# Performance work log

Hardware: AMD Instinct MI355X
Metric: run time of the kernel (lower is better)

The kernel has to match this reference:

```python
import jax, jax.numpy as jnp
import numpy as np

B, C, H, W = 4, 256, 64, 64
C8 = C // 8


def setup_inputs() -> dict:
    key = jax.random.key(0)
    ks = jax.random.split(key, 7)
    return {
        "x": jax.random.normal(ks[0], (B, C, H, W), dtype=jnp.float32),
        "Wq": jax.random.normal(ks[1], (C8, C), dtype=jnp.float32) * 0.05,
        "bq": jax.random.normal(ks[2], (C8,), dtype=jnp.float32) * 0.05,
        "Wk": jax.random.normal(ks[3], (C8, C), dtype=jnp.float32) * 0.05,
        "bk": jax.random.normal(ks[4], (C8,), dtype=jnp.float32) * 0.05,
        "Wv": jax.random.normal(ks[5], (C, C), dtype=jnp.float32) * 0.05,
        "bv": jax.random.normal(ks[6], (C,), dtype=jnp.float32) * 0.05,
        "gamma": jnp.zeros((1,), dtype=jnp.float32),
    }


def reference(x, Wq, bq, Wk, bk, Wv, bv, gamma):
    b, c, h, w = x.shape
    n = h * w
    xf = x.reshape(b, c, n)  # [B, C, N]
    # 1x1 convs == per-pixel linear maps over channels
    q = jnp.einsum('oc,bcn->bon', Wq, xf) + bq[None, :, None]  # [B, C/8, N]
    k = jnp.einsum('oc,bcn->bon', Wk, xf) + bk[None, :, None]  # [B, C/8, N]
    v = jnp.einsum('oc,bcn->bon', Wv, xf) + bv[None, :, None]  # [B, C, N]
    # s[b,i,j] = q_i . k_j ; torch softmax over dim=-2 (the i axis)
    s = jnp.einsum('bci,bcj->bij', q, k)  # [B, N, N]
    attn_T = jax.nn.softmax(s, axis=-2)
    # o[b,c,j] = sum_i v[b,c,i] * attn_T[b,i,j]
    o = jnp.einsum('bci,bij->bcj', v, attn_T)  # [B, C, N]
    return x + gamma[0] * o.reshape(b, c, h, w)
```

## Files before the change

### kernel.cpp

```cpp
#include <hip/hip_runtime.h>
#include <hip/hip_bf16.h>


typedef float  f32x16 __attribute__((ext_vector_type(16)));
typedef float  f32x4  __attribute__((ext_vector_type(4)));
typedef short  s16x8  __attribute__((ext_vector_type(8)));
typedef unsigned int u32;
typedef unsigned int u32x4 __attribute__((ext_vector_type(4)));

__device__ __forceinline__ s16x8 ld16(const ushort* p) {
  return *reinterpret_cast<const s16x8*>(p);
}
__device__ __forceinline__ ushort f2bf(float f) {
  return (ushort)((__float_as_uint(f) + 0x8000u) >> 16);
}
__device__ __forceinline__ u32 cvt_pk_bf16(float lo, float hi) {
  u32 r;
  asm("v_cvt_pk_bf16_f32 %0, %1, %2" : "=v"(r) : "v"(lo), "v"(hi));
  return r;
}

__global__ void wf_kernel(const float* __restrict__ Wq, const float* __restrict__ Wk,
                          const float* __restrict__ Wv,
                          const float* __restrict__ bq, const float* __restrict__ bk,
                          const float* __restrict__ bv, ushort* __restrict__ WF) {
  const int blk = blockIdx.x;
  const int ob = blk / 17, kb = blk % 17;
  const int t = threadIdx.x;
  const int l = t >> 3, e = t & 7;
  const int l31 = l & 31, g = l >> 5;
  const int o = ob * 32 + l31;
  float val;
  if (kb == 16) {
    float bias = (ob == 0) ? bq[l31] : (ob == 1) ? bk[l31] : bv[o - 64];
    val = (g == 0 && e == 0) ? bias : 0.f;
  } else {
    const int c = kb * 16 + (e & 3) + ((e >> 2) << 3) + (g << 2);
    val = (ob == 0) ? Wq[l31 * 256 + c]
        : (ob == 1) ? Wk[l31 * 256 + c]
                    : Wv[(o - 64) * 256 + c];
  }
  WF[((size_t)blk * 64 + l) * 8 + e] = f2bf(val);
}

__global__ __launch_bounds__(640) void proj_kernel(
    const float* __restrict__ x, const ushort* __restrict__ WF,
    ushort* __restrict__ qA, ushort* __restrict__ kB, ushort* __restrict__ vA) {
  __shared__ ushort xbf[17 * 1024];
  __shared__ ushort obuf[20480];
  const int bid = blockIdx.x;
  const int b = bid >> 6, w = bid & 63;
  const int n0 = w << 6;
  const int t = threadIdx.x;

  const float* xb = x + (size_t)(b * 256) * 4096 + n0;
  #pragma unroll
  for (int kk = 0; kk < 7; ++kk) {
    int idx = t + kk * 640;
    if (idx < 4096) {
      int c = idx >> 4, nq = idx & 15;
      f32x4 xv = *reinterpret_cast<const f32x4*>(xb + (size_t)c * 4096 + nq * 4);
      int kb = c >> 4, r = c & 15;
      int gg = (r >> 2) & 1, ee = (r & 3) + ((r >> 3) << 2);
      #pragma unroll
      for (int u = 0; u < 4; ++u) {
        int n = nq * 4 + u;
        xbf[kb * 1024 + ((n >> 5) * 2 + gg) * 256 + (n & 31) * 8 + ee] = f2bf(xv[u]);
      }
    }
  }
  for (int u = t; u < 1024; u += 640) {
    int gg = (u >> 8) & 1, ee = u & 7;
    xbf[16 * 1024 + u] = (gg == 0 && ee == 0) ? (ushort)0x3F80 : (ushort)0;
  }
  __syncthreads();

  const int l = t & 63;
  const int wv = __builtin_amdgcn_readfirstlane(t >> 6);
  const int l31 = l & 31, g = l >> 5;

  s16x8 wf[17];
  #pragma unroll
  for (int kb = 0; kb < 17; ++kb)
    wf[kb] = ld16(WF + ((size_t)(wv * 17 + kb) * 64 + l) * 8);

  f32x16 acc[2];
  #pragma unroll
  for (int nb = 0; nb < 2; ++nb)
    #pragma unroll
    for (int r = 0; r < 16; ++r) acc[nb][r] = 0.f;

  #pragma unroll
  for (int nb = 0; nb < 2; ++nb)
    #pragma unroll
    for (int kb = 0; kb < 17; ++kb)
      acc[nb] = __builtin_amdgcn_mfma_f32_32x32x16_bf16(
          wf[kb], ld16(xbf + kb * 1024 + (nb * 2 + g) * 256 + l31 * 8), acc[nb], 0, 0, 0);

  if (wv < 2) {
    const int obase = wv * 2048;
    #pragma unroll
    for (int nb = 0; nb < 2; ++nb)
      #pragma unroll
      for (int r = 0; r < 16; ++r)
        obuf[obase + (nb * 4 + (r >> 3) * 2 + g) * 256 + l31 * 8 + (r & 3) + (((r >> 2) & 1) << 2)]
            = f2bf(acc[nb][r]);
  } else {
    const int gv = (l31 >> 2) & 1;
    const int ev = (l31 & 3) + (((l31 >> 3) & 1) << 2);
    #pragma unroll
    for (int nb = 0; nb < 2; ++nb) {
      const int fi = (nb * 2 + (l31 >> 4)) * 2 + gv;
      #pragma unroll
      for (int r = 0; r < 16; ++r) {
        const int c = (wv - 2) * 32 + (r & 3) + ((r >> 2) << 3) + (g << 2);
        obuf[4096 + (fi * 256 + c) * 8 + ev] = f2bf(acc[nb][r]);
      }
    }
  }
  __syncthreads();

  const size_t qbase = (size_t)(b * 64 + w) * 2048;
  const size_t vbase = ((size_t)b * 512 + w * 8) * 2048;
  #pragma unroll
  for (int kk = 0; kk < 4; ++kk) {
    int ci = t + kk * 640;
    int off = ci * 8;
    s16x8 val = ld16(obuf + off);
    ushort* dst = (off < 2048) ? (qA + qbase + off)
                : (off < 4096) ? (kB + qbase + off - 2048)
                               : (vA + vbase + off - 4096);
    *reinterpret_cast<s16x8*>(dst) = val;
  }
}

__global__ __launch_bounds__(512, 2) void attn_kernel(
    const ushort* __restrict__ qA, const ushort* __restrict__ kB, const ushort* __restrict__ vA,
    const float* __restrict__ x, const float* __restrict__ gamma, float* __restrict__ out) {
  __shared__ ushort pls[2 * 8 * 2 * 512];
  __shared__ float lsr[4][2][64];
  const int bid = blockIdx.x;
  const int b = bid & 3;
  const int jt = bid >> 2;
  const int j0 = jt << 6;
  const int t = threadIdx.x;
  const int l = t & 63;
  const int wv = __builtin_amdgcn_readfirstlane(t >> 6);
  const int l31 = l & 31, g = l >> 5;
  const float gm = gamma[0];

  if (wv >= 4) {
    const int sw = wv - 4;
    s16x8 kf00, kf01, kf10, kf11;
    {
      const size_t kb0 = (size_t)((b * 64 + jt) * 8 + g) * 256 + l31 * 8;
      kf00 = ld16(kB + kb0);
      kf01 = ld16(kB + kb0 + 512);
      kf10 = ld16(kB + kb0 + 1024);
      kf11 = ld16(kB + kb0 + 1536);
    }
    float lsum0 = 1e-30f, lsum1 = 1e-30f;
    s16x8 qf0, qf1;
    {
      const size_t qb = (size_t)((b * 64 + (sw >> 1)) * 8 + (sw & 1) * 4 + g) * 256 + l31 * 8;
      qf0 = ld16(qA + qb);
      qf1 = ld16(qA + qb + 512);
    }
    for (int reg = 0; reg <= 32; ++reg) {
      if (reg < 32) {
        const int wi = reg, buf = wi & 1;
        f32x16 s0, s1;
        #pragma unroll
        for (int r = 0; r < 16; ++r) { s0[r] = 0.f; s1[r] = 0.f; }
        s0 = __builtin_amdgcn_mfma_f32_32x32x16_bf16(qf0, kf00, s0, 0, 0, 0);
        s0 = __builtin_amdgcn_mfma_f32_32x32x16_bf16(qf1, kf01, s0, 0, 0, 0);
        s1 = __builtin_amdgcn_mfma_f32_32x32x16_bf16(qf0, kf10, s1, 0, 0, 0);
        s1 = __builtin_amdgcn_mfma_f32_32x32x16_bf16(qf1, kf11, s1, 0, 0, 0);
        if (wi < 31) {
          const size_t qb = (size_t)((b * 64 + (wi + 1) * 2 + (sw >> 1)) * 8 + (sw & 1) * 4 + g) * 256 + l31 * 8;
          qf0 = ld16(qA + qb);
          qf1 = ld16(qA + qb + 512);
        }
        float p0[16], p1[16], ls0 = 0.f, ls1 = 0.f;
        #pragma unroll
        for (int r = 0; r < 16; ++r) {
          p0[r] = __builtin_amdgcn_exp2f(__builtin_fmaf(s0[r], 1.4426950408889634f, -24.0f));
          p1[r] = __builtin_amdgcn_exp2f(__builtin_fmaf(s1[r], 1.4426950408889634f, -24.0f));
          ls0 += p0[r];
          ls1 += p1[r];
        }
        lsum0 += ls0;
        lsum1 += ls1;
        u32x4 w00, w01, w10, w11;
        #pragma unroll
        for (int q = 0; q < 4; ++q) {
          w00[q] = cvt_pk_bf16(p0[2 * q],     p0[2 * q + 1]);
          w01[q] = cvt_pk_bf16(p0[8 + 2 * q], p0[8 + 2 * q + 1]);
          w10[q] = cvt_pk_bf16(p1[2 * q],     p1[2 * q + 1]);
          w11[q] = cvt_pk_bf16(p1[8 + 2 * q], p1[8 + 2 * q + 1]);
        }
        ushort* p00 = pls + ((buf * 16 + (2 * sw + 0) * 2 + 0) * 512) + l * 8;
        ushort* p01 = pls + ((buf * 16 + (2 * sw + 1) * 2 + 0) * 512) + l * 8;
        ushort* p10 = pls + ((buf * 16 + (2 * sw + 0) * 2 + 1) * 512) + l * 8;
        ushort* p11 = pls + ((buf * 16 + (2 * sw + 1) * 2 + 1) * 512) + l * 8;
        *reinterpret_cast<s16x8*>(p00) = __builtin_bit_cast(s16x8, w00);
        *reinterpret_cast<s16x8*>(p01) = __builtin_bit_cast(s16x8, w01);
        *reinterpret_cast<s16x8*>(p10) = __builtin_bit_cast(s16x8, w10);
        *reinterpret_cast<s16x8*>(p11) = __builtin_bit_cast(s16x8, w11);
      } else {
        lsr[sw][0][l] = lsum0;
        lsr[sw][1][l] = lsum1;
      }
      asm volatile("s_waitcnt lgkmcnt(0)" ::: "memory");
      __builtin_amdgcn_s_barrier();
      __builtin_amdgcn_sched_barrier(0);
    }
  } else {
    const int pv = wv;
    const ushort* vbase = vA + ((size_t)(b * 512 + g) * 256 + pv * 64 + l31) * 8;
    f32x16 acc[2][2];
    #pragma unroll
    for (int cg = 0; cg < 2; ++cg)
      #pragma unroll
      for (int jb = 0; jb < 2; ++jb)
        #pragma unroll
        for (int r = 0; r < 16; ++r) acc[cg][jb][r] = 0.f;
    s16x8 vf[8][2];
    for (int reg = 0; reg <= 32; ++reg) {
      if (reg == 0) {
        #pragma unroll
        for (int m = 0; m < 8; ++m) {
          vf[m][0] = ld16(vbase + (size_t)m * 4096);
          vf[m][1] = ld16(vbase + (size_t)m * 4096 + 256);
        }
      } else {
        const int wi = reg - 1, buf = wi & 1;
        __builtin_amdgcn_s_setprio(1);
        #pragma unroll
        for (int m = 0; m < 8; ++m) {
          s16x8 pf0 = ld16(pls + ((buf * 16 + m * 2 + 0) * 512) + l * 8);
          s16x8 pf1 = ld16(pls + ((buf * 16 + m * 2 + 1) * 512) + l * 8);
          acc[0][0] = __builtin_amdgcn_mfma_f32_32x32x16_bf16(vf[m][0], pf0, acc[0][0], 0, 0, 0);
          acc[1][0] = __builtin_amdgcn_mfma_f32_32x32x16_bf16(vf[m][1], pf0, acc[1][0], 0, 0, 0);
          acc[0][1] = __builtin_amdgcn_mfma_f32_32x32x16_bf16(vf[m][0], pf1, acc[0][1], 0, 0, 0);
          acc[1][1] = __builtin_amdgcn_mfma_f32_32x32x16_bf16(vf[m][1], pf1, acc[1][1], 0, 0, 0);
          if (reg < 32) {
            vf[m][0] = ld16(vbase + (size_t)(reg * 8 + m) * 4096);
            vf[m][1] = ld16(vbase + (size_t)(reg * 8 + m) * 4096 + 256);
          }
        }
        __builtin_amdgcn_s_setprio(0);
      }
      __builtin_amdgcn_s_barrier();
      __builtin_amdgcn_sched_barrier(0);
    }
    #pragma unroll
    for (int jb = 0; jb < 2; ++jb) {
      float tot = 0.f;
      #pragma unroll
      for (int sw2 = 0; sw2 < 4; ++sw2)
        tot += lsr[sw2][jb][l31] + lsr[sw2][jb][l31 + 32];
      const float sc = gm / tot;
      #pragma unroll
      for (int cg = 0; cg < 2; ++cg) {
        #pragma unroll
        for (int r = 0; r < 16; ++r) {
          const int c = pv * 64 + cg * 32 + (r & 3) + ((r >> 2) << 3) + (g << 2);
          const size_t idx = (size_t)(b * 256 + c) * 4096 + j0 + jb * 32 + l31;
          out[idx] = __builtin_fmaf(sc, acc[cg][jb][r], x[idx]);
        }
      }
    }
  }
}

extern "C" void kernel_launch(void* const* d_in, const int* in_sizes, int n_in,
                              void* d_out, int out_size, void* d_ws, size_t ws_size,
                              hipStream_t stream) {
  const float* x     = (const float*)d_in[0];
  const float* Wq    = (const float*)d_in[1];
  const float* bq    = (const float*)d_in[2];
  const float* Wk    = (const float*)d_in[3];
  const float* bk    = (const float*)d_in[4];
  const float* Wv    = (const float*)d_in[5];
  const float* bv    = (const float*)d_in[6];
  const float* gamma = (const float*)d_in[7];
  float* out = (float*)d_out;

  char* ws = (char*)d_ws;
  ushort* WF = (ushort*)(ws);
  ushort* qA = (ushort*)(ws + 262144);
  ushort* kB = (ushort*)(ws + 262144 + 1048576);
  ushort* vA = (ushort*)(ws + 262144 + 2097152);

  wf_kernel  <<<170, 512, 0, stream>>>(Wq, Wk, Wv, bq, bk, bv, WF);
  proj_kernel<<<256, 640, 0, stream>>>(x, WF, qA, kB, vA);
  attn_kernel<<<256, 512, 0, stream>>>(qA, kB, vA, x, gamma, out);
}
```

Baseline: 63.97 us.

## Prefetch residual x tile into LDS by softmax waves; batch P fragment loads

The softmax-producer waves now load the residual x tile for the block's 64 columns across all 256 channels during the last iterations of their loop and stage it in a new 64KB LDS buffer. The PV waves' epilogue then reads x from LDS instead of issuing strided global loads after the main loop. Separately, all 16 P fragments are loaded from LDS into registers before the MFMA sequence rather than interleaved with it. This hides epilogue global latency behind compute, at the cost of much more LDS per block (which may limit the two-blocks-per-CU occupancy) and higher register pressure.

```diff
diff --git a/kernel.cpp b/kernel.cpp
--- a/kernel.cpp
+++ b/kernel.cpp
@@ -138,7 +138,8 @@
     const ushort* __restrict__ qA, const ushort* __restrict__ kB, const ushort* __restrict__ vA,
     const float* __restrict__ x, const float* __restrict__ gamma, float* __restrict__ out) {
   __shared__ ushort pls[2 * 8 * 2 * 512];
-  __shared__ float lsr[4][2][64];
+  __shared__ float  xls[256 * 64];
+  __shared__ float  lsr[4][2][64];
   const int bid = blockIdx.x;
   const int b = bid & 3;
   const int jt = bid >> 2;
@@ -166,7 +167,21 @@
       qf0 = ld16(qA + qb);
       qf1 = ld16(qA + qb + 512);
     }
+    const float* xrow = x + (size_t)(b * 256) * 4096 + j0 + l;
+    float xr[8];
     for (int reg = 0; reg <= 32; ++reg) {
+      if (reg >= 25) {
+        const int cw0 = (reg - 25) * 32 + sw * 8;
+        #pragma unroll
+        for (int rr = 0; rr < 8; ++rr)
+          xls[(cw0 + rr) * 64 + l] = xr[rr];
+      }
+      if (reg >= 24 && reg < 32) {
+        const int cl0 = (reg - 24) * 32 + sw * 8;
+        #pragma unroll
+        for (int rr = 0; rr < 8; ++rr)
+          xr[rr] = xrow[(size_t)(cl0 + rr) * 4096];
+      }
       if (reg < 32) {
         const int wi = reg, buf = wi & 1;
         f32x16 s0, s1;
@@ -235,15 +250,19 @@
         }
       } else {
         const int wi = reg - 1, buf = wi & 1;
+        s16x8 pf[8][2];
+        #pragma unroll
+        for (int m = 0; m < 8; ++m) {
+          pf[m][0] = ld16(pls + ((buf * 16 + m * 2 + 0) * 512) + l * 8);
+          pf[m][1] = ld16(pls + ((buf * 16 + m * 2 + 1) * 512) + l * 8);
+        }
         __builtin_amdgcn_s_setprio(1);
         #pragma unroll
         for (int m = 0; m < 8; ++m) {
-          s16x8 pf0 = ld16(pls + ((buf * 16 + m * 2 + 0) * 512) + l * 8);
-          s16x8 pf1 = ld16(pls + ((buf * 16 + m * 2 + 1) * 512) + l * 8);
-          acc[0][0] = __builtin_amdgcn_mfma_f32_32x32x16_bf16(vf[m][0], pf0, acc[0][0], 0, 0, 0);
-          acc[1][0] = __builtin_amdgcn_mfma_f32_32x32x16_bf16(vf[m][1], pf0, acc[1][0], 0, 0, 0);
-          acc[0][1] = __builtin_amdgcn_mfma_f32_32x32x16_bf16(vf[m][0], pf1, acc[0][1], 0, 0, 0);
-          acc[1][1] = __builtin_amdgcn_mfma_f32_32x32x16_bf16(vf[m][1], pf1, acc[1][1], 0, 0, 0);
+          acc[0][0] = __builtin_amdgcn_mfma_f32_32x32x16_bf16(vf[m][0], pf[m][0], acc[0][0], 0, 0, 0);
+          acc[1][0] = __builtin_amdgcn_mfma_f32_32x32x16_bf16(vf[m][1], pf[m][0], acc[1][0], 0, 0, 0);
+          acc[0][1] = __builtin_amdgcn_mfma_f32_32x32x16_bf16(vf[m][0], pf[m][1], acc[0][1], 0, 0, 0);
+          acc[1][1] = __builtin_amdgcn_mfma_f32_32x32x16_bf16(vf[m][1], pf[m][1], acc[1][1], 0, 0, 0);
           if (reg < 32) {
             vf[m][0] = ld16(vbase + (size_t)(reg * 8 + m) * 4096);
             vf[m][1] = ld16(vbase + (size_t)(reg * 8 + m) * 4096 + 256);
@@ -267,7 +286,7 @@
         for (int r = 0; r < 16; ++r) {
           const int c = pv * 64 + cg * 32 + (r & 3) + ((r >> 2) << 3) + (g << 2);
           const size_t idx = (size_t)(b * 256 + c) * 4096 + j0 + jb * 32 + l31;
-          out[idx] = __builtin_fmaf(sc, acc[cg][jb][r], x[idx]);
+          out[idx] = __builtin_fmaf(sc, acc[cg][jb][r], xls[c * 64 + jb * 32 + l31]);
         }
       }
     }
```

Result: slower. 66.94 us (+4.6%).

## Split PV accumulation across two waves per channel slice with LDS reduction

Applied to the files above, without the earlier changes.

Raises the attention block from 8 to 12 waves by giving each 64-channel slice of the PV product two waves, each handling half of the m sub-steps. The partial accumulators are combined through LDS (reusing the P buffer) before the epilogue, and softmax waves issue extra barriers to stay in step with the new epilogue barriers. The aim is more MFMA parallelism and latency hiding per block. The cost is extra LDS traffic and barriers in the epilogue, plus tighter register limits from launch bounds of 768 threads with 3 blocks per CU.

```diff
diff --git a/kernel.cpp b/kernel.cpp
--- a/kernel.cpp
+++ b/kernel.cpp
@@ -134,11 +134,11 @@
   }
 }
 
-__global__ __launch_bounds__(512, 2) void attn_kernel(
+__global__ __launch_bounds__(768, 3) void attn_kernel(
     const ushort* __restrict__ qA, const ushort* __restrict__ kB, const ushort* __restrict__ vA,
     const float* __restrict__ x, const float* __restrict__ gamma, float* __restrict__ out) {
   __shared__ ushort pls[2 * 8 * 2 * 512];
-  __shared__ float lsr[4][2][64];
+  __shared__ float  lsr[4][2][64];
   const int bid = blockIdx.x;
   const int b = bid & 3;
   const int jt = bid >> 2;
@@ -149,8 +149,8 @@
   const int l31 = l & 31, g = l >> 5;
   const float gm = gamma[0];
 
-  if (wv >= 4) {
-    const int sw = wv - 4;
+  if (wv >= 8) {
+    const int sw = wv - 8;
     s16x8 kf00, kf01, kf10, kf11;
     {
       const size_t kb0 = (size_t)((b * 64 + jt) * 8 + g) * 256 + l31 * 8;
@@ -215,9 +215,12 @@
       __builtin_amdgcn_s_barrier();
       __builtin_amdgcn_sched_barrier(0);
     }
+    __builtin_amdgcn_s_barrier();
+    __builtin_amdgcn_s_barrier();
+    __builtin_amdgcn_s_barrier();
   } else {
-    const int pv = wv;
-    const ushort* vbase = vA + ((size_t)(b * 512 + g) * 256 + pv * 64 + l31) * 8;
+    const int cs = wv >> 1, mh = wv & 1;
+    const ushort* vbase = vA + ((size_t)(b * 512 + g) * 256 + cs * 64 + l31) * 8;
     f32x16 acc[2][2];
     #pragma unroll
     for (int cg = 0; cg < 2; ++cg)
@@ -225,28 +228,29 @@
       for (int jb = 0; jb < 2; ++jb)
         #pragma unroll
         for (int r = 0; r < 16; ++r) acc[cg][jb][r] = 0.f;
-    s16x8 vf[8][2];
+    s16x8 vf[4][2];
     for (int reg = 0; reg <= 32; ++reg) {
       if (reg == 0) {
         #pragma unroll
-        for (int m = 0; m < 8; ++m) {
-          vf[m][0] = ld16(vbase + (size_t)m * 4096);
-          vf[m][1] = ld16(vbase + (size_t)m * 4096 + 256);
+        for (int u = 0; u < 4; ++u) {
+          vf[u][0] = ld16(vbase + (size_t)(2 * u + mh) * 4096);
+          vf[u][1] = ld16(vbase + (size_t)(2 * u + mh) * 4096 + 256);
         }
       } else {
         const int wi = reg - 1, buf = wi & 1;
         __builtin_amdgcn_s_setprio(1);
         #pragma unroll
-        for (int m = 0; m < 8; ++m) {
+        for (int u = 0; u < 4; ++u) {
+          const int m = 2 * u + mh;
           s16x8 pf0 = ld16(pls + ((buf * 16 + m * 2 + 0) * 512) + l * 8);
           s16x8 pf1 = ld16(pls + ((buf * 16 + m * 2 + 1) * 512) + l * 8);
-          acc[0][0] = __builtin_amdgcn_mfma_f32_32x32x16_bf16(vf[m][0], pf0, acc[0][0], 0, 0, 0);
-          acc[1][0] = __builtin_amdgcn_mfma_f32_32x32x16_bf16(vf[m][1], pf0, acc[1][0], 0, 0, 0);
-          acc[0][1] = __builtin_amdgcn_mfma_f32_32x32x16_bf16(vf[m][0], pf1, acc[0][1], 0, 0, 0);
-          acc[1][1] = __builtin_amdgcn_mfma_f32_32x32x16_bf16(vf[m][1], pf1, acc[1][1], 0, 0, 0);
+          acc[0][0] = __builtin_amdgcn_mfma_f32_32x32x16_bf16(vf[u][0], pf0, acc[0][0], 0, 0, 0);
+          acc[1][0] = __builtin_amdgcn_mfma_f32_32x32x16_bf16(vf[u][1], pf0, acc[1][0], 0, 0, 0);
+          acc[0][1] = __builtin_amdgcn_mfma_f32_32x32x16_bf16(vf[u][0], pf1, acc[0][1], 0, 0, 0);
+          acc[1][1] = __builtin_amdgcn_mfma_f32_32x32x16_bf16(vf[u][1], pf1, acc[1][1], 0, 0, 0);
           if (reg < 32) {
-            vf[m][0] = ld16(vbase + (size_t)(reg * 8 + m) * 4096);
-            vf[m][1] = ld16(vbase + (size_t)(reg * 8 + m) * 4096 + 256);
+            vf[u][0] = ld16(vbase + (size_t)(reg * 8 + m) * 4096);
+            vf[u][1] = ld16(vbase + (size_t)(reg * 8 + m) * 4096 + 256);
           }
         }
         __builtin_amdgcn_s_setprio(0);
@@ -254,21 +258,39 @@
       __builtin_amdgcn_s_barrier();
       __builtin_amdgcn_sched_barrier(0);
     }
+    float* sacc = (float*)pls;
     #pragma unroll
     for (int jb = 0; jb < 2; ++jb) {
       float tot = 0.f;
       #pragma unroll
-      for (int sw2 = 0; sw2 < 4; ++sw2)
-        tot += lsr[sw2][jb][l31] + lsr[sw2][jb][l31 + 32];
+      for (int is2 = 0; is2 < 4; ++is2)
+        tot += lsr[is2][jb][l31] + lsr[is2][jb][l31 + 32];
       const float sc = gm / tot;
-      #pragma unroll
-      for (int cg = 0; cg < 2; ++cg) {
-        #pragma unroll
-        for (int r = 0; r < 16; ++r) {
-          const int c = pv * 64 + cg * 32 + (r & 3) + ((r >> 2) << 3) + (g << 2);
-          const size_t idx = (size_t)(b * 256 + c) * 4096 + j0 + jb * 32 + l31;
-          out[idx] = __builtin_fmaf(sc, acc[cg][jb][r], x[idx]);
-        }
+      if (mh == 0) {
+        #pragma unroll
+        for (int cg = 0; cg < 2; ++cg)
+          #pragma unroll
+          for (int r = 0; r < 16; ++r)
+            sacc[((cs * 2 + cg) * 16 + r) * 64 + l] = acc[cg][jb][r];
+        asm volatile("s_waitcnt lgkmcnt(0)" ::: "memory");
+      }
+      __builtin_amdgcn_s_barrier();
+      __builtin_amdgcn_sched_barrier(0);
+      if (mh == 1) {
+        #pragma unroll
+        for (int cg = 0; cg < 2; ++cg) {
+          #pragma unroll
+          for (int r = 0; r < 16; ++r) {
+            const float o = acc[cg][jb][r] + sacc[((cs * 2 + cg) * 16 + r) * 64 + l];
+            const int c = cs * 64 + cg * 32 + (r & 3) + ((r >> 2) << 3) + (g << 2);
+            const size_t idx = (size_t)(b * 256 + c) * 4096 + j0 + jb * 32 + l31;
+            out[idx] = __builtin_fmaf(sc, o, x[idx]);
+          }
+        }
+      }
+      if (jb == 0) {
+        __builtin_amdgcn_s_barrier();
+        __builtin_amdgcn_sched_barrier(0);
       }
     }
   }
@@ -295,5 +317,5 @@
 
   wf_kernel  <<<170, 512, 0, stream>>>(Wq, Wk, Wv, bq, bk, bv, WF);
   proj_kernel<<<256, 640, 0, stream>>>(x, WF, qA, kB, vA);
-  attn_kernel<<<256, 512, 0, stream>>>(qA, kB, vA, x, gamma, out);
-}
+  attn_kernel<<<256, 768, 0, stream>>>(qA, kB, vA, x, gamma, out);
+}
```

Result: slower. 68.33 us (+6.8%).
